# Optimization experiments

Measured on AMD Instinct MI355X. Metric: run time of the kernel, lower is better.

## Reference

```python
import jax, jax.numpy as jnp
import numpy as np
from jax import lax

EPS = 1e-3  # keras BatchNormalization default epsilon

def _bn(x, g, b, m, v):
    # inference-mode batchnorm over channel axis (last)
    return (x - m) * (g * lax.rsqrt(v + EPS)) + b

def _cond_dw(h, Wdw, bdw, rw):
    # h: [B,H,W,M]; Wdw: [E,3,3,M]; bdw: [E,M]; rw: [B,E]
    E, M = Wdw.shape[0], Wdw.shape[-1]
    out = jnp.zeros_like(h)
    for i in range(E):  # small fixed expert count
        k = Wdw[i].reshape(3, 3, 1, M)  # depthwise kernel, groups=M
        y = lax.conv_general_dilated(
            h, k, window_strides=(1, 1), padding='SAME',
            dimension_numbers=('NHWC', 'HWIO', 'NHWC'),
            feature_group_count=M) + bdw[i]
        out = out + y * rw[:, i, None, None, None]
    return out

def setup_inputs() -> dict:
    key = jax.random.key(0)
    ks = jax.random.split(key, 24)
    B, H, W, C = 32, 56, 56, 96
    E, M, F = 4, 384, 96
    d = {}
    d['x'] = jax.random.normal(ks[0], (B, H, W, C), jnp.float32)
    d['Wr'] = jax.random.normal(ks[1], (C, E), jnp.float32) * 0.1
    d['br'] = jax.random.normal(ks[2], (E,), jnp.float32) * 0.1
    d['Wpw'] = jax.random.normal(ks[3], (E, C, M), jnp.float32) * (2.0 / C) ** 0.5
    d['bpw'] = jax.random.normal(ks[4], (E, M), jnp.float32) * 0.01
    d['Wdw'] = jax.random.normal(ks[5], (E, 3, 3, M), jnp.float32) * 0.1
    d['bdw'] = jax.random.normal(ks[6], (E, M), jnp.float32) * 0.01
    d['Wpwl'] = jax.random.normal(ks[7], (E, M, F), jnp.float32) * (2.0 / M) ** 0.5
    d['bpwl'] = jax.random.normal(ks[8], (E, F), jnp.float32) * 0.01
    d['g1'] = jax.random.uniform(ks[9], (M,), jnp.float32, 0.5, 1.5)
    d['b1'] = jax.random.normal(ks[10], (M,), jnp.float32) * 0.1
    d['m1'] = jax.random.normal(ks[11], (M,), jnp.float32) * 0.1
    d['v1'] = jax.random.uniform(ks[12], (M,), jnp.float32, 0.5, 1.5)
    d['g2'] = jax.random.uniform(ks[13], (M,), jnp.float32, 0.5, 1.5)
    d['b2'] = jax.random.normal(ks[14], (M,), jnp.float32) * 0.1
    d['m2'] = jax.random.normal(ks[15], (M,), jnp.float32) * 0.1
    d['v2'] = jax.random.uniform(ks[16], (M,), jnp.float32, 0.5, 1.5)
    d['g3'] = jax.random.uniform(ks[17], (F,), jnp.float32, 0.5, 1.5)
    d['b3'] = jax.random.normal(ks[18], (F,), jnp.float32) * 0.1
    d['m3'] = jax.random.normal(ks[19], (F,), jnp.float32) * 0.1
    d['v3'] = jax.random.uniform(ks[20], (F,), jnp.float32, 0.5, 1.5)
    return d

def reference(x, Wr, br, Wpw, bpw, Wdw, bdw, Wpwl, bpwl,
              g1, b1, m1, v1, g2, b2, m2, v2, g3, b3, m3, v3):
    shortcut = x
    # routing: global avg pool + dense + sigmoid
    pooled = jnp.mean(x, axis=(1, 2))                      # [B,C]
    rw = jax.nn.sigmoid(pooled @ Wr + br)                  # [B,E]
    # cond pointwise expand: combine 1x1 expert kernels per-sample (linear in kernel)
    Wk = jnp.einsum('be,ecm->bcm', rw, Wpw)
    h = jnp.einsum('bhwc,bcm->bhwm', x, Wk) + (rw @ bpw)[:, None, None, :]
    h = jax.nn.relu(_bn(h, g1, b1, m1, v1))
    # cond depthwise 3x3
    h = _cond_dw(h, Wdw, bdw, rw)
    h = jax.nn.relu(_bn(h, g2, b2, m2, v2))
    # cond pointwise project
    Wk2 = jnp.einsum('be,emf->bmf', rw, Wpwl)
    h = jnp.einsum('bhwm,bmf->bhwf', h, Wk2) + (rw @ bpwl)[:, None, None, :]
    h = _bn(h, g3, b3, m3, v3)
    return h + shortcut
```

## Files before the change

kernel.cpp:

```cpp
#include <hip/hip_runtime.h>

#define B_ 32
#define HH 56
#define WW 56
#define C_ 96
#define E_ 4
#define M_ 384
#define F_ 96
#define P_ 3136
#define EPS 1e-3f

typedef __attribute__((ext_vector_type(8))) __bf16 bf16x8;
typedef __attribute__((ext_vector_type(8))) short short8;
typedef __attribute__((ext_vector_type(4))) float f32x4;
typedef __attribute__((ext_vector_type(2))) float f32x2;
typedef __attribute__((ext_vector_type(4))) unsigned short us4;
typedef unsigned short u16;

__device__ __forceinline__ float bf2f(u16 s) {
  union { unsigned u; float f; } c;
  c.u = ((unsigned)s) << 16;
  return c.f;
}
__device__ __forceinline__ u16 f2bf(float f) {
  union { float f; unsigned u; } c;
  c.f = f;
  unsigned u = c.u + 0x7FFFu + ((c.u >> 16) & 1u);
  return (u16)(u >> 16);
}
__device__ __forceinline__ f32x2 bfpair(unsigned u) {
  union { unsigned i; float f; } lo, hi;
  lo.i = u << 16;
  hi.i = u & 0xffff0000u;
  f32x2 r;
  r.x = lo.f;
  r.y = hi.f;
  return r;
}

__global__ __launch_bounds__(256) void k_pool_convert(
    const float* __restrict__ x, float* __restrict__ partial, u16* __restrict__ xbf) {
  int chunk = blockIdx.x, b = blockIdx.y;
  int p0 = chunk * 49;
  const float* xb = x + ((size_t)b * P_ + p0) * C_;
  u16* xo = xbf + ((size_t)b * P_ + p0) * C_;
  int t = threadIdx.x;
  int c4 = t % 24, s = t / 24;
  __shared__ f32x4 part[10][24];
  if (s < 10) {
    f32x4 sum = {0.f, 0.f, 0.f, 0.f};
    for (int p = s; p < 49; p += 10) {
      f32x4 v = *(const f32x4*)&xb[(size_t)p * C_ + c4 * 4];
      sum += v;
      us4 o;
      o.x = f2bf(v.x); o.y = f2bf(v.y); o.z = f2bf(v.z); o.w = f2bf(v.w);
      *(us4*)&xo[(size_t)p * C_ + c4 * 4] = o;
    }
    part[s][c4] = sum;
  }
  __syncthreads();
  if (s == 0) {
    f32x4 acc = part[0][c4];
#pragma unroll
    for (int ss = 1; ss < 10; ++ss) acc += part[ss][c4];
    *(f32x4*)&partial[(((size_t)b * 64 + chunk)) * C_ + c4 * 4] = acc;
  }
}

__global__ __launch_bounds__(128) void k_routing2(
    const float* __restrict__ partial, const float* __restrict__ Wr,
    const float* __restrict__ br, float* __restrict__ rw) {
  int b = blockIdx.x;
  int c = threadIdx.x;
  __shared__ float pooled[C_];
  if (c < C_) {
    float s = 0.f;
    for (int ch = 0; ch < 64; ++ch) s += partial[((size_t)b * 64 + ch) * C_ + c];
    pooled[c] = s * (1.f / (float)P_);
  }
  __syncthreads();
  if (c < E_) {
    float acc = br[c];
    for (int cc = 0; cc < C_; ++cc) acc += pooled[cc] * Wr[cc * E_ + c];
    rw[b * E_ + c] = 1.f / (1.f + expf(-acc));
  }
}

__global__ __launch_bounds__(256) void k_mkall(
    const float* __restrict__ Wpw, const float* __restrict__ bpw,
    const float* __restrict__ Wdw, const float* __restrict__ bdw,
    const float* __restrict__ Wpwl, const float* __restrict__ bpwl,
    const float* __restrict__ rw,
    const float* __restrict__ g1, const float* __restrict__ b1,
    const float* __restrict__ m1, const float* __restrict__ v1,
    const float* __restrict__ g2, const float* __restrict__ b2,
    const float* __restrict__ m2, const float* __restrict__ v2,
    const float* __restrict__ g3, const float* __restrict__ b3,
    const float* __restrict__ m3, const float* __restrict__ v3,
    u16* __restrict__ Wk_t, float* __restrict__ bias1p,
    float* __restrict__ Wdwf_t,
    u16* __restrict__ Wk2_t, float* __restrict__ bias3p) {
  int b = blockIdx.x, seg = blockIdx.y;
  float r0 = rw[b * 4 + 0], r1 = rw[b * 4 + 1], r2 = rw[b * 4 + 2], r3 = rw[b * 4 + 3];
  int t = threadIdx.x;
  if (seg < 6) {
    __shared__ __align__(16) u16 tile[64][104];
    int ml = t & 63;
    int m = seg * 64 + ml, cp = t >> 6;
    float s1 = g1[m] * rsqrtf(v1[m] + EPS);
#pragma unroll
    for (int j = 0; j < 24; ++j) {
      int c = cp + 4 * j;
      float w = r0 * Wpw[(0 * C_ + c) * M_ + m] + r1 * Wpw[(1 * C_ + c) * M_ + m] +
                r2 * Wpw[(2 * C_ + c) * M_ + m] + r3 * Wpw[(3 * C_ + c) * M_ + m];
      tile[ml][c] = f2bf(w * s1);
    }
    __syncthreads();
    u16* dst = Wk_t + ((size_t)b * M_ + seg * 64) * C_;
#pragma unroll
    for (int k = 0; k < 3; ++k) {
      int ch = t + 256 * k;
      int mr = ch / 12, off = (ch % 12) * 8;
      *(short8*)&dst[(size_t)mr * C_ + off] = *(const short8*)&tile[mr][off];
    }
  } else if (seg == 6) {
    for (int m = t; m < M_; m += 256) {
      float s2 = g2[m] * rsqrtf(v2[m] + EPS);
      int oct = m >> 3, q = m & 7;
      float* base = Wdwf_t + ((size_t)b * 48 + oct) * 80;
#pragma unroll
      for (int tap = 0; tap < 9; ++tap) {
        float w = r0 * Wdw[(0 * 9 + tap) * M_ + m] + r1 * Wdw[(1 * 9 + tap) * M_ + m] +
                  r2 * Wdw[(2 * 9 + tap) * M_ + m] + r3 * Wdw[(3 * 9 + tap) * M_ + m];
        base[tap * 8 + q] = w * s2;
      }
      float bias = r0 * bdw[m] + r1 * bdw[M_ + m] + r2 * bdw[2 * M_ + m] + r3 * bdw[3 * M_ + m];
      base[72 + q] = (bias - m2[m]) * s2 + b2[m];
      float s1 = g1[m] * rsqrtf(v1[m] + EPS);
      float bb = r0 * bpw[m] + r1 * bpw[M_ + m] + r2 * bpw[2 * M_ + m] + r3 * bpw[3 * M_ + m];
      bias1p[b * M_ + m] = (bb - m1[m]) * s1 + b1[m];
    }
    if (t < F_) {
      float s3 = g3[t] * rsqrtf(v3[t] + EPS);
      float bb = r0 * bpwl[t] + r1 * bpwl[F_ + t] + r2 * bpwl[2 * F_ + t] + r3 * bpwl[3 * F_ + t];
      bias3p[b * F_ + t] = (bb - m3[t]) * s3 + b3[t];
    }
  } else {
    __shared__ __align__(16) u16 tile2[96][72];
    int m0 = (seg - 7) * 64;
#pragma unroll
    for (int j = 0; j < 24; ++j) {
      int id = t + 256 * j;
      int m = id / 96, f = id % 96;
      float w = r0 * Wpwl[(0 * M_ + m0 + m) * F_ + f] + r1 * Wpwl[(1 * M_ + m0 + m) * F_ + f] +
                r2 * Wpwl[(2 * M_ + m0 + m) * F_ + f] + r3 * Wpwl[(3 * M_ + m0 + m) * F_ + f];
      float s3 = g3[f] * rsqrtf(v3[f] + EPS);
      tile2[f][m] = f2bf(w * s3);
    }
    __syncthreads();
    u16* dst = Wk2_t + (size_t)b * F_ * M_ + m0;
#pragma unroll
    for (int k = 0; k < 3; ++k) {
      int ch = t + 256 * k;
      int f = ch / 8, off = (ch % 8) * 8;
      *(short8*)&dst[(size_t)f * M_ + off] = *(const short8*)&tile2[f][off];
    }
  }
}

__global__ __launch_bounds__(256) void k_expand(
    const u16* __restrict__ xbf, const u16* __restrict__ Wk_t,
    const float* __restrict__ bias1p, u16* __restrict__ h1b) {
  int pt = blockIdx.x, b = blockIdx.y;
  int p0 = pt * 64;
  int t = threadIdx.x;
  int lane = t & 63, w = t >> 6;
  int r15 = lane & 15, g = lane >> 4;
  int rA = w * 16 + r15;
  int k0 = g * 8;
  const u16* A = xbf + ((size_t)b * P_ + p0) * C_;
  bf16x8 af[3];
#pragma unroll
  for (int kc = 0; kc < 3; ++kc)
    af[kc] = *(const bf16x8*)&A[(size_t)rA * C_ + kc * 32 + k0];
  const u16* Bt = Wk_t + (size_t)b * M_ * C_;
  u16* outb = h1b + (size_t)b * 48 * P_ * 8;
  int rowb = p0 + w * 16 + g * 4;
  for (int nt = 0; nt < 6; ++nt) {
    f32x4 acc[4] = {};
#pragma unroll
    for (int kc = 0; kc < 3; ++kc) {
#pragma unroll
      for (int ct = 0; ct < 4; ++ct) {
        bf16x8 bb = *(const bf16x8*)
            &Bt[(size_t)(nt * 64 + ct * 16 + r15) * C_ + kc * 32 + k0];
        acc[ct] = __builtin_amdgcn_mfma_f32_16x16x32_bf16(af[kc], bb, acc[ct], 0, 0, 0);
      }
    }
#pragma unroll
    for (int ct = 0; ct < 4; ++ct) {
      int m = nt * 64 + ct * 16 + r15;
      int oct = m >> 3, q = m & 7;
      float bias = bias1p[b * M_ + m];
#pragma unroll
      for (int i = 0; i < 4; ++i) {
        float v = fmaxf(acc[ct][i] + bias, 0.f);
        outb[((size_t)oct * P_ + rowb + i) * 8 + q] = f2bf(v);
      }
    }
  }
}

__global__ __launch_bounds__(512) void k_dw(
    const u16* __restrict__ h1b, const float* __restrict__ Wdwf_t,
    u16* __restrict__ h2b) {
  int oct = blockIdx.x, b = blockIdx.y;
  int t = threadIdx.x;
  __shared__ uint4 tile[58 * 58];

  int wbase = __builtin_amdgcn_readfirstlane((b * 48 + oct) * 80);
  const float* wo = Wdwf_t + wbase;
  f32x2 w2[40];
#pragma unroll
  for (int i = 0; i < 40; ++i) w2[i] = *(const f32x2*)&wo[i * 2];

  const uint4* in = (const uint4*)(h1b + ((size_t)b * 48 + oct) * P_ * 8);
  uint4* outb = (uint4*)(h2b + ((size_t)b * 48 + oct) * P_ * 8);

  uint4 z = {0u, 0u, 0u, 0u};
  if (t < 58) { tile[t] = z; tile[57 * 58 + t] = z; }
  else if (t < 114) { int s = t - 58; tile[(s + 1) * 58] = z; tile[(s + 1) * 58 + 57] = z; }
  for (int j = t; j < P_; j += 512) {
    int yy = j / 56, xx = j % 56;
    tile[(yy + 1) * 58 + xx + 1] = in[j];
  }
  __syncthreads();

  for (int i = t; i < P_; i += 512) {
    int y = i / 56, x = i % 56;
    f32x2 acc[4] = {w2[36], w2[37], w2[38], w2[39]};
#pragma unroll
    for (int dy = 0; dy < 3; ++dy) {
#pragma unroll
      for (int dx = 0; dx < 3; ++dx) {
        uint4 u = tile[(y + dy) * 58 + (x + dx)];
        int tap = dy * 3 + dx;
        acc[0] += bfpair(u.x) * w2[tap * 4 + 0];
        acc[1] += bfpair(u.y) * w2[tap * 4 + 1];
        acc[2] += bfpair(u.z) * w2[tap * 4 + 2];
        acc[3] += bfpair(u.w) * w2[tap * 4 + 3];
      }
    }
    unsigned o[4];
#pragma unroll
    for (int j = 0; j < 4; ++j) {
      float lo = fmaxf(acc[j].x, 0.f), hi = fmaxf(acc[j].y, 0.f);
      asm("v_cvt_pk_bf16_f32 %0, %1, %2" : "=v"(o[j]) : "v"(lo), "v"(hi));
    }
    uint4 st = {o[0], o[1], o[2], o[3]};
    outb[i] = st;
  }
}

__global__ __launch_bounds__(256) void k_proj(
    const u16* __restrict__ h2b, const u16* __restrict__ Wk2_t,
    const float* __restrict__ bias3p, const u16* __restrict__ xbf,
    float* __restrict__ outp) {
  __shared__ __align__(16) u16 As[64][104];
  __shared__ __align__(16) u16 Bs[96][104];
  int pt = blockIdx.x, b = blockIdx.y;
  int p0 = pt * 64;
  int t = threadIdx.x;
  const u16* h2base = h2b + (size_t)b * 48 * P_ * 8;
  const u16* Bt = Wk2_t + (size_t)b * F_ * M_;
  int lane = t & 63, w = t >> 6;
  int rA = w * 16 + (lane & 15);
  int k0 = (lane >> 4) * 8;
  f32x4 acc[6] = {};
  for (int kc = 0; kc < 4; ++kc) {
    if (kc) __syncthreads();
#pragma unroll
    for (int j = 0; j < 3; ++j) {
      int ch = t + 256 * j;
      int r = ch / 12, ol = ch % 12;
      *(short8*)&As[r][ol * 8] =
          *(const short8*)&h2base[((size_t)(kc * 12 + ol) * P_ + p0 + r) * 8];
    }
#pragma unroll
    for (int j = 0; j < 5; ++j) {
      int ch = t + 256 * j;
      if (ch < 96 * 12) {
        int r = ch / 12, o = (ch % 12) * 8;
        *(short8*)&Bs[r][o] = *(const short8*)&Bt[(size_t)r * M_ + kc * 96 + o];
      }
    }
    __syncthreads();
#pragma unroll
    for (int ks = 0; ks < 3; ++ks) {
      bf16x8 a = *(const bf16x8*)&As[rA][ks * 32 + k0];
#pragma unroll
      for (int ct = 0; ct < 6; ++ct) {
        bf16x8 bb = *(const bf16x8*)&Bs[ct * 16 + (lane & 15)][ks * 32 + k0];
        acc[ct] = __builtin_amdgcn_mfma_f32_16x16x32_bf16(a, bb, acc[ct], 0, 0, 0);
      }
    }
  }
  const u16* xr = xbf + (size_t)b * P_ * C_;
  float* op = outp + (size_t)b * P_ * F_;
  int rowb = p0 + w * 16 + (lane >> 4) * 4;
#pragma unroll
  for (int ct = 0; ct < 6; ++ct) {
    int f = ct * 16 + (lane & 15);
    float bias = bias3p[b * F_ + f];
#pragma unroll
    for (int i = 0; i < 4; ++i) {
      size_t idx = (size_t)(rowb + i) * F_ + f;
      op[idx] = acc[ct][i] + bias + bf2f(xr[idx]);
    }
  }
}

extern "C" void kernel_launch(void* const* d_in, const int* in_sizes, int n_in,
                              void* d_out, int out_size, void* d_ws, size_t ws_size,
                              hipStream_t stream) {
  (void)in_sizes; (void)n_in; (void)out_size; (void)ws_size;
  const float* x    = (const float*)d_in[0];
  const float* Wr   = (const float*)d_in[1];
  const float* br   = (const float*)d_in[2];
  const float* Wpw  = (const float*)d_in[3];
  const float* bpw  = (const float*)d_in[4];
  const float* Wdw  = (const float*)d_in[5];
  const float* bdw  = (const float*)d_in[6];
  const float* Wpwl = (const float*)d_in[7];
  const float* bpwl = (const float*)d_in[8];
  const float* g1 = (const float*)d_in[9];
  const float* b1 = (const float*)d_in[10];
  const float* m1 = (const float*)d_in[11];
  const float* v1 = (const float*)d_in[12];
  const float* g2 = (const float*)d_in[13];
  const float* b2 = (const float*)d_in[14];
  const float* m2 = (const float*)d_in[15];
  const float* v2 = (const float*)d_in[16];
  const float* g3 = (const float*)d_in[17];
  const float* b3 = (const float*)d_in[18];
  const float* m3 = (const float*)d_in[19];
  const float* v3 = (const float*)d_in[20];
  float* out = (float*)d_out;

  char* p = (char*)d_ws;
  auto alloc = [&](size_t bytes) {
    char* r = p;
    p += (bytes + 255) & ~(size_t)255;
    return r;
  };
  float* rw      = (float*)alloc((size_t)B_ * E_ * 4);
  float* partial = (float*)alloc((size_t)B_ * 64 * C_ * 4);
  u16*   xbf     = (u16*)  alloc((size_t)B_ * P_ * C_ * 2);
  u16*   Wk_t    = (u16*)  alloc((size_t)B_ * M_ * C_ * 2);
  float* bias1p  = (float*)alloc((size_t)B_ * M_ * 4);
  float* Wdwf_t  = (float*)alloc((size_t)B_ * 48 * 80 * 4);
  u16*   Wk2_t   = (u16*)  alloc((size_t)B_ * F_ * M_ * 2);
  float* bias3p  = (float*)alloc((size_t)B_ * F_ * 4);
  u16*   h1b     = (u16*)  alloc((size_t)B_ * P_ * M_ * 2);
  u16*   h2b     = (u16*)  alloc((size_t)B_ * P_ * M_ * 2);

  k_pool_convert<<<dim3(64, B_), 256, 0, stream>>>(x, partial, xbf);
  k_routing2<<<B_, 128, 0, stream>>>(partial, Wr, br, rw);
  k_mkall<<<dim3(B_, 13), 256, 0, stream>>>(Wpw, bpw, Wdw, bdw, Wpwl, bpwl, rw,
                                            g1, b1, m1, v1, g2, b2, m2, v2,
                                            g3, b3, m3, v3,
                                            Wk_t, bias1p, Wdwf_t, Wk2_t, bias3p);
  k_expand<<<dim3(49, B_), 256, 0, stream>>>(xbf, Wk_t, bias1p, h1b);
  k_dw<<<dim3(48, B_), 512, 0, stream>>>(h1b, Wdwf_t, h2b);
  k_proj<<<dim3(49, B_), 256, 0, stream>>>(h2b, Wk2_t, bias3p, xbf, out);
}
```

Measured before the change: 150.6 us.

## Switch intermediates to planar/NHWC layouts and give each wave a 64-row GEMM tile

The expand GEMM now writes h1 in channel-planar layout with packed bf16 stores. The depthwise kernel tiles channel groups by 14-row strips, transposing into LDS and writing h2 in NHWC. The expand and projection GEMMs give each wave a 64-row tile (four MFMA fragments) and read operands straight from global memory, dropping LDS staging and block syncs. The goal is better operand reuse and coalesced intermediate traffic. The cost is fewer blocks (13 per batch, last block partly idle), higher register pressure, and strided uncoalesced A-fragment loads in proj.

```diff
diff --git a/kernel.cpp b/kernel.cpp
--- a/kernel.cpp
+++ b/kernel.cpp
@@ -35,6 +35,11 @@
   f32x2 r;
   r.x = lo.f;
   r.y = hi.f;
+  return r;
+}
+__device__ __forceinline__ unsigned pkbf(float a, float b) {
+  unsigned r;
+  asm("v_cvt_pk_bf16_f32 %0, %1, %2" : "=v"(r) : "v"(a), "v"(b));
   return r;
 }
 
@@ -126,16 +131,15 @@
   } else if (seg == 6) {
     for (int m = t; m < M_; m += 256) {
       float s2 = g2[m] * rsqrtf(v2[m] + EPS);
-      int oct = m >> 3, q = m & 7;
-      float* base = Wdwf_t + ((size_t)b * 48 + oct) * 80;
+      float* base = Wdwf_t + ((size_t)b * M_ + m) * 10;
 #pragma unroll
       for (int tap = 0; tap < 9; ++tap) {
         float w = r0 * Wdw[(0 * 9 + tap) * M_ + m] + r1 * Wdw[(1 * 9 + tap) * M_ + m] +
                   r2 * Wdw[(2 * 9 + tap) * M_ + m] + r3 * Wdw[(3 * 9 + tap) * M_ + m];
-        base[tap * 8 + q] = w * s2;
+        base[tap] = w * s2;
       }
       float bias = r0 * bdw[m] + r1 * bdw[M_ + m] + r2 * bdw[2 * M_ + m] + r3 * bdw[3 * M_ + m];
-      base[72 + q] = (bias - m2[m]) * s2 + b2[m];
+      base[9] = (bias - m2[m]) * s2 + b2[m];
       float s1 = g1[m] * rsqrtf(v1[m] + EPS);
       float bb = r0 * bpw[m] + r1 * bpw[M_ + m] + r2 * bpw[2 * M_ + m] + r3 * bpw[3 * M_ + m];
       bias1p[b * M_ + m] = (bb - m1[m]) * s1 + b1[m];
@@ -170,152 +174,168 @@
 
 __global__ __launch_bounds__(256) void k_expand(
     const u16* __restrict__ xbf, const u16* __restrict__ Wk_t,
-    const float* __restrict__ bias1p, u16* __restrict__ h1b) {
-  int pt = blockIdx.x, b = blockIdx.y;
-  int p0 = pt * 64;
-  int t = threadIdx.x;
-  int lane = t & 63, w = t >> 6;
+    const float* __restrict__ bias1p, u16* __restrict__ h1) {
+  int b = blockIdx.y;
+  int t = threadIdx.x;
+  int w = t >> 6, lane = t & 63;
+  int wid = blockIdx.x * 4 + w;
+  if (wid >= 49) return;
   int r15 = lane & 15, g = lane >> 4;
-  int rA = w * 16 + r15;
+  int r0 = wid * 64;
   int k0 = g * 8;
-  const u16* A = xbf + ((size_t)b * P_ + p0) * C_;
-  bf16x8 af[3];
-#pragma unroll
-  for (int kc = 0; kc < 3; ++kc)
-    af[kc] = *(const bf16x8*)&A[(size_t)rA * C_ + kc * 32 + k0];
+  const u16* A = xbf + (size_t)b * P_ * C_;
+  bf16x8 af[4][3];
+#pragma unroll
+  for (int fr = 0; fr < 4; ++fr)
+#pragma unroll
+    for (int kc = 0; kc < 3; ++kc)
+      af[fr][kc] = *(const bf16x8*)&A[(size_t)(r0 + fr * 16 + r15) * C_ + kc * 32 + k0];
   const u16* Bt = Wk_t + (size_t)b * M_ * C_;
-  u16* outb = h1b + (size_t)b * 48 * P_ * 8;
-  int rowb = p0 + w * 16 + g * 4;
+  u16* h1b = h1 + (size_t)b * M_ * P_;
   for (int nt = 0; nt < 6; ++nt) {
-    f32x4 acc[4] = {};
+    f32x4 acc[4][4] = {};
 #pragma unroll
     for (int kc = 0; kc < 3; ++kc) {
 #pragma unroll
       for (int ct = 0; ct < 4; ++ct) {
         bf16x8 bb = *(const bf16x8*)
             &Bt[(size_t)(nt * 64 + ct * 16 + r15) * C_ + kc * 32 + k0];
-        acc[ct] = __builtin_amdgcn_mfma_f32_16x16x32_bf16(af[kc], bb, acc[ct], 0, 0, 0);
+#pragma unroll
+        for (int fr = 0; fr < 4; ++fr)
+          acc[ct][fr] = __builtin_amdgcn_mfma_f32_16x16x32_bf16(af[fr][kc], bb, acc[ct][fr], 0, 0, 0);
       }
     }
 #pragma unroll
     for (int ct = 0; ct < 4; ++ct) {
       int m = nt * 64 + ct * 16 + r15;
-      int oct = m >> 3, q = m & 7;
       float bias = bias1p[b * M_ + m];
-#pragma unroll
-      for (int i = 0; i < 4; ++i) {
-        float v = fmaxf(acc[ct][i] + bias, 0.f);
-        outb[((size_t)oct * P_ + rowb + i) * 8 + q] = f2bf(v);
-      }
-    }
-  }
-}
-
-__global__ __launch_bounds__(512) void k_dw(
-    const u16* __restrict__ h1b, const float* __restrict__ Wdwf_t,
-    u16* __restrict__ h2b) {
-  int oct = blockIdx.x, b = blockIdx.y;
-  int t = threadIdx.x;
-  __shared__ uint4 tile[58 * 58];
-
-  int wbase = __builtin_amdgcn_readfirstlane((b * 48 + oct) * 80);
-  const float* wo = Wdwf_t + wbase;
-  f32x2 w2[40];
-#pragma unroll
-  for (int i = 0; i < 40; ++i) w2[i] = *(const f32x2*)&wo[i * 2];
-
-  const uint4* in = (const uint4*)(h1b + ((size_t)b * 48 + oct) * P_ * 8);
-  uint4* outb = (uint4*)(h2b + ((size_t)b * 48 + oct) * P_ * 8);
-
-  uint4 z = {0u, 0u, 0u, 0u};
-  if (t < 58) { tile[t] = z; tile[57 * 58 + t] = z; }
-  else if (t < 114) { int s = t - 58; tile[(s + 1) * 58] = z; tile[(s + 1) * 58 + 57] = z; }
-  for (int j = t; j < P_; j += 512) {
-    int yy = j / 56, xx = j % 56;
-    tile[(yy + 1) * 58 + xx + 1] = in[j];
+      u16* plane = h1b + (size_t)m * P_;
+#pragma unroll
+      for (int fr = 0; fr < 4; ++fr) {
+        int p = r0 + fr * 16 + g * 4;
+        float v0 = fmaxf(acc[ct][fr][0] + bias, 0.f);
+        float v1 = fmaxf(acc[ct][fr][1] + bias, 0.f);
+        float v2 = fmaxf(acc[ct][fr][2] + bias, 0.f);
+        float v3 = fmaxf(acc[ct][fr][3] + bias, 0.f);
+        uint2 st = {pkbf(v0, v1), pkbf(v2, v3)};
+        *(uint2*)&plane[p] = st;
+      }
+    }
+  }
+}
+
+__global__ __launch_bounds__(256) void k_dw(
+    const u16* __restrict__ h1, const float* __restrict__ Wdwf,
+    u16* __restrict__ h2) {
+  int cg = blockIdx.x;
+  int strip = blockIdx.y;
+  int b = blockIdx.z;
+  int m0 = cg * 32, y0 = strip * 14;
+  int t = threadIdx.x;
+  __shared__ __align__(16) u16 inT[16 * 58 * 40];
+  if (t < 32) {
+    int yl = t >> 1, xl = (t & 1) * 57;
+    uint4 z4 = {0u, 0u, 0u, 0u};
+#pragma unroll
+    for (int c8 = 0; c8 < 4; ++c8)
+      *(uint4*)&inT[(yl * 58 + xl) * 40 + c8 * 8] = z4;
+  }
+  const u16* src = h1 + (size_t)b * M_ * P_;
+#pragma unroll
+  for (int j = 0; j < 14; ++j) {
+    int cid = t + 256 * j;
+    int o = cid % 7;
+    int yl = (cid / 7) % 16;
+    int c = cid / 112;
+    int yg = y0 - 1 + yl;
+    short8 v = {0, 0, 0, 0, 0, 0, 0, 0};
+    if ((unsigned)yg < 56u)
+      v = *(const short8*)&src[(size_t)(m0 + c) * P_ + yg * 56 + o * 8];
+#pragma unroll
+    for (int k = 0; k < 8; ++k)
+      inT[(yl * 58 + o * 8 + k + 1) * 40 + c] = (u16)v[k];
   }
   __syncthreads();
-
-  for (int i = t; i < P_; i += 512) {
-    int y = i / 56, x = i % 56;
-    f32x2 acc[4] = {w2[36], w2[37], w2[38], w2[39]};
+  int cp = t & 15, pi = t >> 4;
+  int c0 = m0 + cp * 2;
+  const float* wa = Wdwf + ((size_t)b * M_ + c0) * 10;
+  f32x2 wv[9], bias2;
+#pragma unroll
+  for (int tap = 0; tap < 9; ++tap) {
+    wv[tap].x = wa[tap];
+    wv[tap].y = wa[10 + tap];
+  }
+  bias2.x = wa[9];
+  bias2.y = wa[19];
+  u16* dst = h2 + (size_t)b * P_ * M_;
+  for (int j = 0; j < 49; ++j) {
+    int p = pi + 16 * j;
+    int y = p / 56, x = p % 56;
+    f32x2 acc = bias2;
 #pragma unroll
     for (int dy = 0; dy < 3; ++dy) {
 #pragma unroll
       for (int dx = 0; dx < 3; ++dx) {
-        uint4 u = tile[(y + dy) * 58 + (x + dx)];
-        int tap = dy * 3 + dx;
-        acc[0] += bfpair(u.x) * w2[tap * 4 + 0];
-        acc[1] += bfpair(u.y) * w2[tap * 4 + 1];
-        acc[2] += bfpair(u.z) * w2[tap * 4 + 2];
-        acc[3] += bfpair(u.w) * w2[tap * 4 + 3];
-      }
-    }
-    unsigned o[4];
-#pragma unroll
-    for (int j = 0; j < 4; ++j) {
-      float lo = fmaxf(acc[j].x, 0.f), hi = fmaxf(acc[j].y, 0.f);
-      asm("v_cvt_pk_bf16_f32 %0, %1, %2" : "=v"(o[j]) : "v"(lo), "v"(hi));
-    }
-    uint4 st = {o[0], o[1], o[2], o[3]};
-    outb[i] = st;
+        unsigned u = *(const unsigned*)&inT[((y + dy) * 58 + x + dx) * 40 + cp * 2];
+        acc += bfpair(u) * wv[dy * 3 + dx];
+      }
+    }
+    unsigned r = pkbf(fmaxf(acc.x, 0.f), fmaxf(acc.y, 0.f));
+    int pg = (y0 + y) * 56 + x;
+    *(unsigned*)&dst[(size_t)pg * M_ + c0] = r;
   }
 }
 
 __global__ __launch_bounds__(256) void k_proj(
-    const u16* __restrict__ h2b, const u16* __restrict__ Wk2_t,
+    const u16* __restrict__ h2, const u16* __restrict__ Wk2_t,
     const float* __restrict__ bias3p, const u16* __restrict__ xbf,
     float* __restrict__ outp) {
-  __shared__ __align__(16) u16 As[64][104];
-  __shared__ __align__(16) u16 Bs[96][104];
-  int pt = blockIdx.x, b = blockIdx.y;
-  int p0 = pt * 64;
-  int t = threadIdx.x;
-  const u16* h2base = h2b + (size_t)b * 48 * P_ * 8;
+  int b = blockIdx.y;
+  int t = threadIdx.x;
+  int w = t >> 6, lane = t & 63;
+  int wid = blockIdx.x * 4 + w;
+  if (wid >= 49) return;
+  int r15 = lane & 15, g = lane >> 4;
+  int r0 = wid * 64;
+  int k0 = g * 8;
+  const u16* A = h2 + (size_t)b * P_ * M_;
   const u16* Bt = Wk2_t + (size_t)b * F_ * M_;
-  int lane = t & 63, w = t >> 6;
-  int rA = w * 16 + (lane & 15);
-  int k0 = (lane >> 4) * 8;
-  f32x4 acc[6] = {};
+  f32x4 acc[6][4] = {};
+#pragma unroll 1
   for (int kc = 0; kc < 4; ++kc) {
-    if (kc) __syncthreads();
-#pragma unroll
-    for (int j = 0; j < 3; ++j) {
-      int ch = t + 256 * j;
-      int r = ch / 12, ol = ch % 12;
-      *(short8*)&As[r][ol * 8] =
-          *(const short8*)&h2base[((size_t)(kc * 12 + ol) * P_ + p0 + r) * 8];
-    }
-#pragma unroll
-    for (int j = 0; j < 5; ++j) {
-      int ch = t + 256 * j;
-      if (ch < 96 * 12) {
-        int r = ch / 12, o = (ch % 12) * 8;
-        *(short8*)&Bs[r][o] = *(const short8*)&Bt[(size_t)r * M_ + kc * 96 + o];
-      }
-    }
-    __syncthreads();
+    bf16x8 af[4][3];
+#pragma unroll
+    for (int fr = 0; fr < 4; ++fr)
+#pragma unroll
+      for (int ks = 0; ks < 3; ++ks)
+        af[fr][ks] = *(const bf16x8*)
+            &A[(size_t)(r0 + fr * 16 + r15) * M_ + kc * 96 + ks * 32 + k0];
 #pragma unroll
     for (int ks = 0; ks < 3; ++ks) {
-      bf16x8 a = *(const bf16x8*)&As[rA][ks * 32 + k0];
 #pragma unroll
       for (int ct = 0; ct < 6; ++ct) {
-        bf16x8 bb = *(const bf16x8*)&Bs[ct * 16 + (lane & 15)][ks * 32 + k0];
-        acc[ct] = __builtin_amdgcn_mfma_f32_16x16x32_bf16(a, bb, acc[ct], 0, 0, 0);
+        bf16x8 bb = *(const bf16x8*)
+            &Bt[(size_t)(ct * 16 + r15) * M_ + kc * 96 + ks * 32 + k0];
+#pragma unroll
+        for (int fr = 0; fr < 4; ++fr)
+          acc[ct][fr] = __builtin_amdgcn_mfma_f32_16x16x32_bf16(af[fr][ks], bb, acc[ct][fr], 0, 0, 0);
       }
     }
   }
   const u16* xr = xbf + (size_t)b * P_ * C_;
   float* op = outp + (size_t)b * P_ * F_;
-  int rowb = p0 + w * 16 + (lane >> 4) * 4;
 #pragma unroll
   for (int ct = 0; ct < 6; ++ct) {
-    int f = ct * 16 + (lane & 15);
+    int f = ct * 16 + r15;
     float bias = bias3p[b * F_ + f];
 #pragma unroll
-    for (int i = 0; i < 4; ++i) {
-      size_t idx = (size_t)(rowb + i) * F_ + f;
-      op[idx] = acc[ct][i] + bias + bf2f(xr[idx]);
+    for (int fr = 0; fr < 4; ++fr) {
+#pragma unroll
+      for (int i = 0; i < 4; ++i) {
+        int p = r0 + fr * 16 + g * 4 + i;
+        size_t idx = (size_t)p * F_ + f;
+        op[idx] = acc[ct][fr][i] + bias + bf2f(xr[idx]);
+      }
     }
   }
 }
@@ -358,11 +378,11 @@
   u16*   xbf     = (u16*)  alloc((size_t)B_ * P_ * C_ * 2);
   u16*   Wk_t    = (u16*)  alloc((size_t)B_ * M_ * C_ * 2);
   float* bias1p  = (float*)alloc((size_t)B_ * M_ * 4);
-  float* Wdwf_t  = (float*)alloc((size_t)B_ * 48 * 80 * 4);
+  float* Wdwf_t  = (float*)alloc((size_t)B_ * M_ * 10 * 4);
   u16*   Wk2_t   = (u16*)  alloc((size_t)B_ * F_ * M_ * 2);
   float* bias3p  = (float*)alloc((size_t)B_ * F_ * 4);
-  u16*   h1b     = (u16*)  alloc((size_t)B_ * P_ * M_ * 2);
-  u16*   h2b     = (u16*)  alloc((size_t)B_ * P_ * M_ * 2);
+  u16*   h1      = (u16*)  alloc((size_t)B_ * M_ * P_ * 2);
+  u16*   h2      = (u16*)  alloc((size_t)B_ * P_ * M_ * 2);
 
   k_pool_convert<<<dim3(64, B_), 256, 0, stream>>>(x, partial, xbf);
   k_routing2<<<B_, 128, 0, stream>>>(partial, Wr, br, rw);
@@ -370,7 +390,7 @@
                                             g1, b1, m1, v1, g2, b2, m2, v2,
                                             g3, b3, m3, v3,
                                             Wk_t, bias1p, Wdwf_t, Wk2_t, bias3p);
-  k_expand<<<dim3(49, B_), 256, 0, stream>>>(xbf, Wk_t, bias1p, h1b);
-  k_dw<<<dim3(48, B_), 512, 0, stream>>>(h1b, Wdwf_t, h2b);
-  k_proj<<<dim3(49, B_), 256, 0, stream>>>(h2b, Wk2_t, bias3p, xbf, out);
-}
+  k_expand<<<dim3(13, B_), 256, 0, stream>>>(xbf, Wk_t, bias1p, h1);
+  k_dw<<<dim3(12, 4, B_), 256, 0, stream>>>(h1, Wdwf_t, h2);
+  k_proj<<<dim3(13, B_), 256, 0, stream>>>(h2, Wk2_t, bias3p, xbf, out);
+}
```

After: 170.3 us. 13.1% more time.
